# Kernel optimization log

Measured on AMD Instinct MI355X. Metric: run time of the kernel, lower is better.

The kernel has to match this reference:

```python
import jax, jax.numpy as jnp
import numpy as np

NEG_INF = -9e15
LEAKY_SLOPE = 0.2  # init alpha
N, IN_DIM, OUT_DIM = 8192, 512, 256


def setup_inputs() -> dict:
    key = jax.random.key(0)
    k1, k2, k3, k4, k5 = jax.random.split(key, 5)
    h = jax.random.normal(k1, (N, IN_DIM), dtype=jnp.float32)
    adj = jax.random.randint(k2, (N, N), 0, 2, dtype=jnp.int32)
    W = jax.random.normal(k3, (IN_DIM, OUT_DIM), dtype=jnp.float32) * 0.06
    a_left = jax.random.normal(k4, (OUT_DIM, 1), dtype=jnp.float32) * 0.1
    a_right = jax.random.normal(k5, (OUT_DIM, 1), dtype=jnp.float32) * 0.1
    return {"h": h, "adj": adj, "W": W, "a_left": a_left, "a_right": a_right}


def reference(h, adj, W, a_left, a_right):
    Wh = h @ W                                  # [N, out_dim]
    Wh1 = Wh @ a_left                           # [N, 1]
    Wh2 = Wh @ a_right                          # [N, 1]
    e = Wh1 + Wh2.T                             # [N, N] broadcast additive scores
    e = jnp.where(e > 0, e, LEAKY_SLOPE * e)    # LeakyReLU
    e = jnp.where(adj > 0, e, NEG_INF)          # adjacency mask
    attention = jax.nn.softmax(e, axis=1)       # row-wise softmax (dropout=0, eval)
    h_out = attention @ Wh                      # [N, out_dim]
    return jax.nn.elu(h_out)                    # activation=True
```

## Files before the change

### kernel.cpp

```cpp
#include <hip/hip_runtime.h>
#include <hip/hip_bf16.h>
#include <cstdint>
#include <cstddef>

typedef float  f32x4  __attribute__((ext_vector_type(4)));
typedef __bf16 bf16x8 __attribute__((ext_vector_type(8)));

#define LOG2E 1.4426950408889634f

static constexpr int GN   = 8192;
static constexpr int GIN  = 512;
static constexpr int GOUT = 256;

static __device__ __forceinline__ void gload_lds16(const void* g, void* lds){
  typedef uint32_t __attribute__((address_space(1)))* gp_t;
  typedef uint32_t __attribute__((address_space(3)))* lp_t;
  __builtin_amdgcn_global_load_lds((gp_t)(uintptr_t)g,
                                   (lp_t)(uint32_t)(uintptr_t)lds, 16, 0, 0);
}

__global__ __launch_bounds__(256) void k_pre1(const float* __restrict__ W,
                                              const float* __restrict__ al,
                                              const float* __restrict__ ar,
                                              const float* __restrict__ h,
                                              float* __restrict__ wal,
                                              float* __restrict__ war,
                                              __bf16* __restrict__ WT,
                                              __bf16* __restrict__ hb){
  __shared__ float T[64][65];
  const int bid = blockIdx.x, tid = threadIdx.x;
  if(bid < 128){
    const int k = bid*4 + (tid>>6), lane = tid & 63;
    float4 wv = ((const float4*)(W + (size_t)k*GOUT))[lane];
    float4 av = ((const float4*)al)[lane];
    float4 bv = ((const float4*)ar)[lane];
    float sl = wv.x*av.x + wv.y*av.y + wv.z*av.z + wv.w*av.w;
    float sr = wv.x*bv.x + wv.y*bv.y + wv.z*bv.z + wv.w*bv.w;
    #pragma unroll
    for(int o=32;o;o>>=1){ sl += __shfl_down(sl,o,64); sr += __shfl_down(sr,o,64); }
    if(lane==0){ wal[k] = sl*LOG2E; war[k] = sr*LOG2E; }
  } else if(bid < 160){
    const int tile = bid - 128;
    const int k0 = (tile>>2)*64, c0 = (tile&3)*64;
    const int r = tid>>2, cs = (tid&3)*16;
    #pragma unroll
    for(int j=0;j<4;j++){
      float4 v = *(const float4*)(W + (size_t)(k0+r)*GOUT + c0 + cs + 4*j);
      T[r][cs+4*j+0]=v.x; T[r][cs+4*j+1]=v.y; T[r][cs+4*j+2]=v.z; T[r][cs+4*j+3]=v.w;
    }
    __syncthreads();
    bf16x8 o1, o2;
    #pragma unroll
    for(int j=0;j<8;j++){ o1[j]=(__bf16)T[cs+j][r]; o2[j]=(__bf16)T[cs+8+j][r]; }
    __bf16* dst = WT + (size_t)(c0+r)*GIN + k0 + cs;
    *(bf16x8*)dst = o1;
    *(bf16x8*)(dst+8) = o2;
  } else {
    size_t i = ((size_t)(bid-160)*256 + tid)*8;
    float4 v0 = *(const float4*)(h+i);
    float4 v1 = *(const float4*)(h+i+4);
    bf16x8 o;
    o[0]=(__bf16)v0.x; o[1]=(__bf16)v0.y; o[2]=(__bf16)v0.z; o[3]=(__bf16)v0.w;
    o[4]=(__bf16)v1.x; o[5]=(__bf16)v1.y; o[6]=(__bf16)v1.z; o[7]=(__bf16)v1.w;
    *(bf16x8*)(hb+i) = o;
  }
}

__global__ __launch_bounds__(256) void k_pre2(const __bf16* __restrict__ WT,
                                              const __bf16* __restrict__ hb,
                                              __bf16* __restrict__ WhbT,
                                              const float* __restrict__ h,
                                              const float* __restrict__ wal,
                                              const float* __restrict__ war,
                                              float* __restrict__ Wh1,
                                              float* __restrict__ Wh2){
  __shared__ __attribute__((aligned(16))) __bf16 As[2][64*64];
  __shared__ __attribute__((aligned(16))) __bf16 Bs[2][128*64];
  const int bid = blockIdx.x, tid = threadIdx.x;
  const int lane = tid & 63, w = tid >> 6;

  if(bid < 256){
    const int mb = bid >> 6, nb = bid & 63;
    const int m0 = mb*64, n0 = nb*128;

    f32x4 acc[8];
    #pragma unroll
    for(int t=0;t<8;t++) acc[t] = (f32x4){0.f,0.f,0.f,0.f};

    const int lr = lane>>3;
    const int bs_sw = ((lane&7)*16) ^ (lr<<4);

    auto stage = [&](int it, int buf){
      const int k0b = it*128;
      #pragma unroll
      for(int s=0;s<6;s++){
        int u = w + s*4;
        const char* src; char* dst;
        if(u < 8){
          int r8 = u*8;
          src = (const char*)(WT + (size_t)(m0 + r8 + lr)*GIN);
          dst = (char*)&As[buf][0] + r8*128;
        } else {
          int r8 = (u-8)*8;
          src = (const char*)(hb + (size_t)(n0 + r8 + lr)*GIN);
          dst = (char*)&Bs[buf][0] + r8*128;
        }
        gload_lds16(src + k0b + bs_sw, dst);
      }
    };

    auto kstep = [&](int kk, int buf){
      const int ko = kk*64 + (lane>>4)*16;
      const int am = 16*w + (lane&15);
      bf16x8 af = *(const bf16x8*)((const char*)&As[buf][0] + am*128 + (ko ^ ((am&7)<<4)));
      #pragma unroll
      for(int t=0;t<8;t++){
        int n = 16*t + (lane&15);
        bf16x8 bf = *(const bf16x8*)((const char*)&Bs[buf][0] + n*128 + (ko ^ ((n&7)<<4)));
        acc[t] = __builtin_amdgcn_mfma_f32_16x16x32_bf16(af, bf, acc[t], 0, 0, 0);
      }
    };

    stage(0,0);
    asm volatile("s_waitcnt vmcnt(0)" ::: "memory");
    __builtin_amdgcn_s_barrier();
    for(int it=0; it<8; it++){
      int buf = it & 1;
      if(it < 7) stage(it+1, buf^1);
      kstep(0, buf);
      kstep(1, buf);
      asm volatile("s_waitcnt vmcnt(0)" ::: "memory");
      __builtin_amdgcn_s_barrier();
    }

    const int mrow = m0 + 16*w + 4*(lane>>4);
    const int nc0  = n0 + (lane&15);
    #pragma unroll
    for(int t=0;t<8;t++){
      #pragma unroll
      for(int r=0;r<4;r++){
        WhbT[(size_t)(mrow + r)*GN + nc0 + 16*t] = (__bf16)acc[t][r];
      }
    }
  } else {
    const int row = (bid-256)*4 + w;
    const float4* hp = (const float4*)(h + (size_t)row*GIN);
    float4 v0 = hp[lane*2], v1 = hp[lane*2+1];
    float4 a0 = ((const float4*)wal)[lane*2], a1 = ((const float4*)wal)[lane*2+1];
    float4 b0 = ((const float4*)war)[lane*2], b1 = ((const float4*)war)[lane*2+1];
    float sl = v0.x*a0.x+v0.y*a0.y+v0.z*a0.z+v0.w*a0.w
             + v1.x*a1.x+v1.y*a1.y+v1.z*a1.z+v1.w*a1.w;
    float sr = v0.x*b0.x+v0.y*b0.y+v0.z*b0.z+v0.w*b0.w
             + v1.x*b1.x+v1.y*b1.y+v1.z*b1.z+v1.w*b1.w;
    #pragma unroll
    for(int of=32;of;of>>=1){ sl += __shfl_down(sl,of,64); sr += __shfl_down(sr,of,64); }
    if(lane==0){ Wh1[row]=sl; Wh2[row]=sr; }
  }
}

template<bool PART>
__global__ __launch_bounds__(256,2) void k_attn(const int* __restrict__ adj,
                                                const __bf16* __restrict__ WhbT,
                                                const float* __restrict__ Wh1s,
                                                const float* __restrict__ Wh2s,
                                                float* __restrict__ pv_out,
                                                float* __restrict__ s_out){
  __shared__ __attribute__((aligned(16))) char Vs[2][16384];
  __shared__ __attribute__((aligned(16))) unsigned int mkL[32*128];
  __shared__ __attribute__((aligned(16))) float wh2L[1024];
  const int tid = threadIdx.x, lane = tid & 63, w = tid >> 6;
  const int rg = blockIdx.x >> 3, chunk = blockIdx.x & 7;
  const int r0 = rg * 128;
  const int j0 = chunk * 1024;
  const int la = lane & 15, kg = lane >> 4, kg8 = kg << 3;

  float4 wv = *(const float4*)(Wh2s + j0 + tid*4);
  const float wh1_0 = Wh1s[r0 + 16*w + la];
  const float wh1_1 = Wh1s[r0 + 16*w + la + 64];

  const int l_log = (lane&7) ^ (lane>>3);
  const char* wbase = (const char*)WhbT
                    + (size_t)(64*w + 2*(lane>>3) + (l_log>>2))*(GN*2)
                    + (size_t)(l_log&3)*16;
  auto stage = [&](int it, int buf){
    const size_t colb = (size_t)(j0 + it*32)*2;
    char* dst = &Vs[buf][0] + w*4096 + lane*16;
    #pragma unroll
    for(int s=0;s<4;s++){
      gload_lds16(wbase + (size_t)(16*s)*(GN*2) + colb, dst + s*1024);
    }
  };

  stage(0, 0);

  {
    const size_t abase = (size_t)(r0 + 32*w)*GN + j0;
    const int idx = lane & 31;
    const int shift = (idx & 7) * 8;
    const bool qb0 = (idx >> 3) & 1, qb1 = (idx >> 4) & 1;
    int4 A0[4], A1[4];
    auto rload = [&](int r, int4 (&A)[4]){
      const int* p = adj + abase + (size_t)r*GN + lane*4;
      #pragma unroll
      for(int q=0;q<4;q++) A[q] = *(const int4*)(p + q*256);
    };
    auto rpack = [&](int r, int4 (&A)[4]){
      uint64_t B00 = __ballot(A[0].x!=0), B01 = __ballot(A[0].y!=0),
               B02 = __ballot(A[0].z!=0), B03 = __ballot(A[0].w!=0);
      uint64_t B10 = __ballot(A[1].x!=0), B11 = __ballot(A[1].y!=0),
               B12 = __ballot(A[1].z!=0), B13 = __ballot(A[1].w!=0);
      uint64_t B20 = __ballot(A[2].x!=0), B21 = __ballot(A[2].y!=0),
               B22 = __ballot(A[2].z!=0), B23 = __ballot(A[2].w!=0);
      uint64_t B30 = __ballot(A[3].x!=0), B31 = __ballot(A[3].y!=0),
               B32 = __ballot(A[3].z!=0), B33 = __ballot(A[3].w!=0);
      uint64_t u0 = qb1 ? (qb0? B30:B20) : (qb0? B10:B00);
      uint64_t u1 = qb1 ? (qb0? B31:B21) : (qb0? B11:B01);
      uint64_t u2 = qb1 ? (qb0? B32:B22) : (qb0? B12:B02);
      uint64_t u3 = qb1 ? (qb0? B33:B23) : (qb0? B13:B03);
      unsigned int word = ((unsigned int)(u0 >> shift) & 0xffu)
                        | (((unsigned int)(u1 >> shift) & 0xffu) << 8)
                        | (((unsigned int)(u2 >> shift) & 0xffu) << 16)
                        | (((unsigned int)(u3 >> shift) & 0xffu) << 24);
      if(lane < 32){
        const int row = 32*w + r;
        mkL[idx*128 + (row ^ idx)] = word;
      }
    };
    rload(0, A0);
    #pragma unroll 1
    for(int rp=0; rp<16; ++rp){
      const int ra = 2*rp, rb = ra+1;
      rload(rb, A1);
      rpack(ra, A0);
      if(rp < 15) rload(rb+1, A0);
      rpack(rb, A1);
    }
  }

  *(float4*)&wh2L[tid*4] = wv;

  f32x4 acc0[16], acc1[16];
  #pragma unroll
  for(int t=0;t<16;t++){ acc0[t] = (f32x4){0.f,0.f,0.f,0.f}; acc1[t] = (f32x4){0.f,0.f,0.f,0.f}; }
  f32x4 accs0 = (f32x4){0.f,0.f,0.f,0.f};
  f32x4 accs1 = (f32x4){0.f,0.f,0.f,0.f};
  bf16x8 ones;
  #pragma unroll
  for(int j=0;j<8;j++) ones[j] = (__bf16)1.0f;

  __syncthreads();

  auto mkpa = [&](float wh1, unsigned mm, float4 w0, float4 w1) -> bf16x8 {
    bf16x8 pa;
    float y, p;
    y = wh1 + w0.x; y = fmaxf(y, 0.2f*y); p = exp2f(y); pa[0] = (__bf16)((mm    )&1 ? p : 0.f);
    y = wh1 + w0.y; y = fmaxf(y, 0.2f*y); p = exp2f(y); pa[1] = (__bf16)((mm>>8 )&1 ? p : 0.f);
    y = wh1 + w0.z; y = fmaxf(y, 0.2f*y); p = exp2f(y); pa[2] = (__bf16)((mm>>16)&1 ? p : 0.f);
    y = wh1 + w0.w; y = fmaxf(y, 0.2f*y); p = exp2f(y); pa[3] = (__bf16)((mm>>24)&1 ? p : 0.f);
    y = wh1 + w1.x; y = fmaxf(y, 0.2f*y); p = exp2f(y); pa[4] = (__bf16)((mm>>1 )&1 ? p : 0.f);
    y = wh1 + w1.y; y = fmaxf(y, 0.2f*y); p = exp2f(y); pa[5] = (__bf16)((mm>>9 )&1 ? p : 0.f);
    y = wh1 + w1.z; y = fmaxf(y, 0.2f*y); p = exp2f(y); pa[6] = (__bf16)((mm>>17)&1 ? p : 0.f);
    y = wh1 + w1.w; y = fmaxf(y, 0.2f*y); p = exp2f(y); pa[7] = (__bf16)((mm>>25)&1 ? p : 0.f);
    return pa;
  };

  const int rd_off = (la>>1)*128 + (((((la&1)<<2) | kg) ^ (la>>1)) << 4);
  const int kg2 = 2*kg;

  auto kstep = [&](int it, int buf){
    unsigned int m0 = mkL[it*128 + ((16*w + la) ^ it)];
    unsigned int m1 = mkL[it*128 + ((16*w + la + 64) ^ it)];
    const float* wp = &wh2L[it*32 + kg8];
    float4 w0 = *(const float4*)wp;
    float4 w1 = *(const float4*)(wp + 4);
    bf16x8 pa0 = mkpa(wh1_0, m0 >> kg2, w0, w1);
    bf16x8 pa1 = mkpa(wh1_1, m1 >> kg2, w0, w1);
    const char* vb = &Vs[buf][0] + rd_off;
    #pragma unroll
    for(int t=0;t<16;t++){
      bf16x8 bv = *(const bf16x8*)(vb + t*1024);
      acc0[t] = __builtin_amdgcn_mfma_f32_16x16x32_bf16(pa0, bv, acc0[t], 0, 0, 0);
      acc1[t] = __builtin_amdgcn_mfma_f32_16x16x32_bf16(pa1, bv, acc1[t], 0, 0, 0);
    }
    accs0 = __builtin_amdgcn_mfma_f32_16x16x32_bf16(pa0, ones, accs0, 0, 0, 0);
    accs1 = __builtin_amdgcn_mfma_f32_16x16x32_bf16(pa1, ones, accs1, 0, 0, 0);
  };

  for(int it=0; it<32; it++){
    const int buf = it & 1;
    if(it < 31) stage(it+1, buf^1);
    kstep(it, buf);
    asm volatile("s_waitcnt vmcnt(0)" ::: "memory");
    __builtin_amdgcn_s_barrier();
  }

  const int orow0 = r0 + 16*w + 4*kg;
  const int orow1 = orow0 + 64;
  const int ocol  = la;
  if constexpr (PART){
    float* pv = pv_out + (size_t)chunk*GN*GOUT;
    float* sp = s_out  + (size_t)chunk*GN;
    #pragma unroll
    for(int t=0;t<16;t++){
      #pragma unroll
      for(int r=0;r<4;r++){
        pv[(size_t)(orow0 + r)*GOUT + ocol + 16*t] = acc0[t][r];
        pv[(size_t)(orow1 + r)*GOUT + ocol + 16*t] = acc1[t][r];
      }
    }
    if(ocol == 0){
      #pragma unroll
      for(int r=0;r<4;r++){ sp[orow0 + r] = accs0[r]; sp[orow1 + r] = accs1[r]; }
    }
  } else {
    #pragma unroll
    for(int t=0;t<16;t++){
      #pragma unroll
      for(int r=0;r<4;r++){
        atomicAdd(pv_out + (size_t)(orow0 + r)*GOUT + ocol + 16*t, acc0[t][r]);
        atomicAdd(pv_out + (size_t)(orow1 + r)*GOUT + ocol + 16*t, acc1[t][r]);
      }
    }
    if(ocol == 0){
      #pragma unroll
      for(int r=0;r<4;r++){ atomicAdd(s_out + orow0 + r, accs0[r]); atomicAdd(s_out + orow1 + r, accs1[r]); }
    }
  }
}

static __device__ __forceinline__ float elu1(float x){
  return x > 0.f ? x : (exp2f(x*LOG2E) - 1.f);
}

__global__ void k_reduce(const float* __restrict__ accP, const float* __restrict__ accSp,
                         float* __restrict__ out){
  size_t i = ((size_t)blockIdx.x*256 + threadIdx.x)*4;
  int row = (int)(i >> 8);
  float S = 0.f;
  #pragma unroll
  for(int c=0;c<8;c++) S += accSp[(size_t)c*GN + row];
  float4 s = {0.f,0.f,0.f,0.f};
  #pragma unroll
  for(int c=0;c<8;c++){
    float4 v = *(const float4*)(accP + (size_t)c*GN*GOUT + i);
    s.x += v.x; s.y += v.y; s.z += v.z; s.w += v.w;
  }
  float inv = 1.0f / S;
  float4 o;
  o.x = elu1(s.x*inv); o.y = elu1(s.y*inv); o.z = elu1(s.z*inv); o.w = elu1(s.w*inv);
  *(float4*)(out + i) = o;
}

__global__ void k_norm(const float* __restrict__ accPV, const float* __restrict__ accS,
                       float* __restrict__ out){
  size_t i = ((size_t)blockIdx.x*256 + threadIdx.x)*4;
  int row = (int)(i >> 8);
  float inv = 1.0f / accS[row];
  float4 v = *(const float4*)(accPV + i);
  float4 o;
  o.x = elu1(v.x*inv); o.y = elu1(v.y*inv); o.z = elu1(v.z*inv); o.w = elu1(v.w*inv);
  *(float4*)(out + i) = o;
}

extern "C" void kernel_launch(void* const* d_in, const int* in_sizes, int n_in,
                              void* d_out, int out_size, void* d_ws, size_t ws_size,
                              hipStream_t stream){
  const float* h  = (const float*)d_in[0];
  const int*   adj= (const int*)  d_in[1];
  const float* W  = (const float*)d_in[2];
  const float* al = (const float*)d_in[3];
  const float* ar = (const float*)d_in[4];
  float* out = (float*)d_out;
  char* ws = (char*)d_ws;

  const size_t SZ_ACCP = (size_t)8*GN*GOUT*4;
  const size_t NEED_A  = SZ_ACCP + 4194304 + 32768 + 32768 + 262144;

  if(ws_size >= NEED_A){
    float*  accP  = (float*) (ws);
    __bf16* hb    = (__bf16*)(ws);
    __bf16* WT    = (__bf16*)(ws + 8388608);
    float*  wal   = (float*) (ws + 8650752);
    float*  war   = (float*) (ws + 8652800);
    __bf16* WhbT  = (__bf16*)(ws + SZ_ACCP);
    float*  Wh1   = (float*) (ws + SZ_ACCP + 4194304);
    float*  Wh2   = (float*) (ws + SZ_ACCP + 4227072);
    float*  accSp = (float*) (ws + SZ_ACCP + 4259840);

    k_pre1<<<2208, 256, 0, stream>>>(W, al, ar, h, wal, war, WT, hb);
    k_pre2<<<2304, 256, 0, stream>>>(WT, hb, WhbT, h, wal, war, Wh1, Wh2);
    k_attn<true><<<512, 256, 0, stream>>>(adj, WhbT, Wh1, Wh2, accP, accSp);
    k_reduce<<<2048, 256, 0, stream>>>(accP, accSp, out);
  } else {
    float*  accPV = (float*) (ws);
    float*  accS  = (float*) (ws + 8388608);
    __bf16* hb    = (__bf16*)(ws + 8421376);
    __bf16* WT    = (__bf16*)(ws + 16809984);
    __bf16* WhbT  = (__bf16*)(ws + 17072128);
    float*  wal   = (float*) (ws + 21266432);
    float*  war   = (float*) (ws + 21268480);
    float*  Wh1   = (float*) (ws + 21270528);
    float*  Wh2   = (float*) (ws + 21303296);
    if(ws_size < 21336064) return;

    hipMemsetAsync(accPV, 0, 8388608 + 32768, stream);
    k_pre1<<<2208, 256, 0, stream>>>(W, al, ar, h, wal, war, WT, hb);
    k_pre2<<<2304, 256, 0, stream>>>(WT, hb, WhbT, h, wal, war, Wh1, Wh2);
    k_attn<false><<<512, 256, 0, stream>>>(adj, WhbT, Wh1, Wh2, accPV, accS);
    k_norm<<<2048, 256, 0, stream>>>(accPV, accS, out);
  }
}
```

Measured before the change: 129.8 us.

## Overlap second half of adjacency bitmask packing with main MFMA loop

The adjacency mask preload is split into two column halves. Only the first half is packed before the main loop. The second half is loaded and ballot-packed during the first 16 iterations, whose kstep reads only first-half mask words. The end-of-iteration wait is relaxed to vmcnt(4), so the in-flight adjacency loads do not block the barrier. This is meant to hide part of the serial prologue's global-memory latency behind MFMA work, at the cost of extra registers and more complex wait-count reasoning in the hot loop.

```diff
diff --git a/kernel.cpp b/kernel.cpp
--- a/kernel.cpp
+++ b/kernel.cpp
@@ -193,47 +193,43 @@
 
   stage(0, 0);
 
+  const size_t abase = (size_t)(r0 + 32*w)*GN + j0;
+  const int idx = lane & 31;
+  const int shift = (idx & 7) * 8;
+  const bool qb0 = (idx >> 3) & 1;
+
+  auto rload2 = [&](int r, int half, int4 (&A)[2]){
+    const int* p = adj + abase + (size_t)r*GN + lane*4 + half*512;
+    A[0] = *(const int4*)(p);
+    A[1] = *(const int4*)(p + 256);
+  };
+  auto rpack2 = [&](int r, int ph, int4 (&A)[2]){
+    uint64_t B00 = __ballot(A[0].x!=0), B01 = __ballot(A[0].y!=0),
+             B02 = __ballot(A[0].z!=0), B03 = __ballot(A[0].w!=0);
+    uint64_t B10 = __ballot(A[1].x!=0), B11 = __ballot(A[1].y!=0),
+             B12 = __ballot(A[1].z!=0), B13 = __ballot(A[1].w!=0);
+    uint64_t u0 = qb0? B10:B00, u1 = qb0? B11:B01;
+    uint64_t u2 = qb0? B12:B02, u3 = qb0? B13:B03;
+    unsigned int word = ((unsigned int)(u0 >> shift) & 0xffu)
+                      | (((unsigned int)(u1 >> shift) & 0xffu) << 8)
+                      | (((unsigned int)(u2 >> shift) & 0xffu) << 16)
+                      | (((unsigned int)(u3 >> shift) & 0xffu) << 24);
+    if(lane < 32 && (lane >> 4) == ph){
+      const int row = 32*w + r;
+      mkL[idx*128 + (row ^ idx)] = word;
+    }
+  };
+
   {
-    const size_t abase = (size_t)(r0 + 32*w)*GN + j0;
-    const int idx = lane & 31;
-    const int shift = (idx & 7) * 8;
-    const bool qb0 = (idx >> 3) & 1, qb1 = (idx >> 4) & 1;
-    int4 A0[4], A1[4];
-    auto rload = [&](int r, int4 (&A)[4]){
-      const int* p = adj + abase + (size_t)r*GN + lane*4;
-      #pragma unroll
-      for(int q=0;q<4;q++) A[q] = *(const int4*)(p + q*256);
-    };
-    auto rpack = [&](int r, int4 (&A)[4]){
-      uint64_t B00 = __ballot(A[0].x!=0), B01 = __ballot(A[0].y!=0),
-               B02 = __ballot(A[0].z!=0), B03 = __ballot(A[0].w!=0);
-      uint64_t B10 = __ballot(A[1].x!=0), B11 = __ballot(A[1].y!=0),
-               B12 = __ballot(A[1].z!=0), B13 = __ballot(A[1].w!=0);
-      uint64_t B20 = __ballot(A[2].x!=0), B21 = __ballot(A[2].y!=0),
-               B22 = __ballot(A[2].z!=0), B23 = __ballot(A[2].w!=0);
-      uint64_t B30 = __ballot(A[3].x!=0), B31 = __ballot(A[3].y!=0),
-               B32 = __ballot(A[3].z!=0), B33 = __ballot(A[3].w!=0);
-      uint64_t u0 = qb1 ? (qb0? B30:B20) : (qb0? B10:B00);
-      uint64_t u1 = qb1 ? (qb0? B31:B21) : (qb0? B11:B01);
-      uint64_t u2 = qb1 ? (qb0? B32:B22) : (qb0? B12:B02);
-      uint64_t u3 = qb1 ? (qb0? B33:B23) : (qb0? B13:B03);
-      unsigned int word = ((unsigned int)(u0 >> shift) & 0xffu)
-                        | (((unsigned int)(u1 >> shift) & 0xffu) << 8)
-                        | (((unsigned int)(u2 >> shift) & 0xffu) << 16)
-                        | (((unsigned int)(u3 >> shift) & 0xffu) << 24);
-      if(lane < 32){
-        const int row = 32*w + r;
-        mkL[idx*128 + (row ^ idx)] = word;
-      }
-    };
-    rload(0, A0);
+    int4 A0[2], A1[2];
+    rload2(0, 0, A0);
     #pragma unroll 1
     for(int rp=0; rp<16; ++rp){
       const int ra = 2*rp, rb = ra+1;
-      rload(rb, A1);
-      rpack(ra, A0);
-      if(rp < 15) rload(rb+1, A0);
-      rpack(rb, A1);
+      rload2(rb, 0, A1);
+      rpack2(ra, 0, A0);
+      if(rp < 15) rload2(rb+1, 0, A0);
+      rpack2(rb, 0, A1);
     }
   }
 
@@ -247,6 +243,10 @@
   bf16x8 ones;
   #pragma unroll
   for(int j=0;j<8;j++) ones[j] = (__bf16)1.0f;
+
+  int4 B0[2], B1[2];
+  rload2(0, 1, B0);
+  rload2(1, 1, B1);
 
   __syncthreads();
 
@@ -286,11 +286,26 @@
     accs1 = __builtin_amdgcn_mfma_f32_16x16x32_bf16(pa1, ones, accs1, 0, 0, 0);
   };
 
+  #pragma unroll 1
   for(int it=0; it<32; it++){
     const int buf = it & 1;
     if(it < 31) stage(it+1, buf^1);
+    if(it < 16){
+      rpack2(2*it,   1, B0);
+      rpack2(2*it+1, 1, B1);
+      if(it < 15){
+        rload2(2*it+2, 1, B0);
+        rload2(2*it+3, 1, B1);
+      }
+    }
     kstep(it, buf);
-    asm volatile("s_waitcnt vmcnt(0)" ::: "memory");
+    if(it < 15){
+      asm volatile("s_waitcnt vmcnt(4)" ::: "memory");
+    } else if(it == 15){
+      asm volatile("s_waitcnt vmcnt(0) lgkmcnt(0)" ::: "memory");
+    } else {
+      asm volatile("s_waitcnt vmcnt(0)" ::: "memory");
+    }
     __builtin_amdgcn_s_barrier();
   }
 
```

Result: no change. 130.4 us (+0.5%).
